# Kernel optimization log

Measured on AMD Instinct MI355X. Metric: run time of the kernel, lower is better.

Reference implementation:

```python
import jax, jax.numpy as jnp
import numpy as np

H = 512      # hidden_size
E = 300      # embed_size
V = 50257    # output_size / vocab
B = 64       # batch
S = 128      # src_len
NEG = -1e10


def setup_inputs() -> dict:
    key = jax.random.key(0)
    ks = jax.random.split(key, 12)
    inp = {
        "input_ids": jax.random.randint(ks[0], (B,), 0, V),
        "hidden": jax.random.normal(ks[1], (B, H), jnp.float32),
        "encoder_outputs": jax.random.normal(ks[2], (S, B, 2 * H), jnp.float32),
        "mask": jax.random.randint(ks[3], (B, S), 0, 2).astype(jnp.int32),
        # parameters
        "emb_table": jax.random.normal(ks[4], (V, E), jnp.float32) * 0.02,
        "W_attn": jax.random.normal(ks[5], (H, 3 * H), jnp.float32) * 0.02,
        "b_attn": jnp.zeros((H,), jnp.float32),
        "v_w": jax.random.normal(ks[6], (1, H), jnp.float32) * 0.02,
        "W_ih": jax.random.normal(ks[7], (3 * H, 2 * H + E), jnp.float32) * 0.02,
        "W_hh": jax.random.normal(ks[8], (3 * H, H), jnp.float32) * 0.02,
        "b_ih": jnp.zeros((3 * H,), jnp.float32),
        "b_hh": jnp.zeros((3 * H,), jnp.float32),
        "W_out": jax.random.normal(ks[9], (V, 3 * H + E), jnp.float32) * 0.02,
        "b_out": jnp.zeros((V,), jnp.float32),
    }
    return inp


def reference(input_ids, hidden, encoder_outputs, mask,
              emb_table, W_attn, b_attn, v_w,
              W_ih, W_hh, b_ih, b_hh, W_out, b_out):
    # embedding lookup (dropout prob = 0 -> identity)
    embedded = emb_table[input_ids]                       # [B, E]

    # Bahdanau attention
    enc_b = jnp.transpose(encoder_outputs, (1, 0, 2))     # [B, S, 2H]
    hid_rep = jnp.broadcast_to(hidden[:, None, :], (hidden.shape[0], enc_b.shape[1], hidden.shape[1]))
    energy = jnp.tanh(jnp.concatenate([hid_rep, enc_b], axis=2) @ W_attn.T + b_attn)  # [B, S, H]
    scores = jnp.einsum('bsh,h->bs', energy, v_w[0])      # [B, S]
    scores = jnp.where(mask == 0, NEG, scores)
    a = jax.nn.softmax(scores, axis=1)                    # [B, S]

    # context vector
    weighted = jnp.einsum('bs,bse->be', a, enc_b)         # [B, 2H]

    # single-step GRU (PyTorch gate order: r, z, n)
    x = jnp.concatenate([embedded, weighted], axis=1)     # [B, E + 2H]
    gx = x @ W_ih.T + b_ih                                # [B, 3H]
    gh = hidden @ W_hh.T + b_hh                           # [B, 3H]
    h = hidden.shape[1]
    r = jax.nn.sigmoid(gx[:, :h] + gh[:, :h])
    z = jax.nn.sigmoid(gx[:, h:2*h] + gh[:, h:2*h])
    n = jnp.tanh(gx[:, 2*h:] + r * gh[:, 2*h:])
    h_new = (1.0 - z) * n + z * hidden                    # [B, H]

    # output projection
    prediction = jnp.concatenate([h_new, weighted, embedded], axis=1) @ W_out.T + b_out  # [B, V]
    return prediction, h_new, a
```

## Files before the change

### kernel.cpp

```cpp
#include <hip/hip_runtime.h>

typedef unsigned short ushort_t;
typedef short bf16x8 __attribute__((ext_vector_type(8)));
typedef float f32x4 __attribute__((ext_vector_type(4)));

#define B_ 64
#define H_ 512
#define E_ 300
#define V_ 50257
#define S_ 128

#define PRED_OFS 0
#define HNEW_OFS ((size_t)64 * 50257)
#define A_OFS    ((size_t)64 * 50257 + 64 * 512)

__device__ __forceinline__ float b2f(unsigned short h) {
  unsigned int u = ((unsigned int)h) << 16;
  return __builtin_bit_cast(float, u);
}
__device__ __forceinline__ unsigned short f2b(float f) {
  unsigned int u = __builtin_bit_cast(unsigned int, f);
  u = u + 0x7FFFu + ((u >> 16) & 1u);
  return (unsigned short)(u >> 16);
}
__device__ __forceinline__ float fast_tanh(float x) {
  x = fminf(15.f, fmaxf(-15.f, x));
  float e = __expf(-2.f * x);
  return (1.f - e) / (1.f + e);
}
__device__ __forceinline__ float fast_sigmoid(float x) {
  return 1.f / (1.f + __expf(-x));
}

template <int DT>
__device__ __forceinline__ ushort4 ldb4(const void* p, size_t off) {
  if constexpr (DT == 0) {
    return *(const ushort4*)((const ushort_t*)p + off);
  } else {
    float4 f = *(const float4*)((const float*)p + off);
    return make_ushort4(f2b(f.x), f2b(f.y), f2b(f.z), f2b(f.w));
  }
}
template <int DT>
__device__ __forceinline__ float lde1(const void* p, size_t off) {
  if constexpr (DT == 0) return b2f(((const ushort_t*)p)[off]);
  else return ((const float*)p)[off];
}
template <int DT>
__device__ __forceinline__ void st1(void* p, size_t off, float v) {
  if constexpr (DT == 0) ((ushort_t*)p)[off] = f2b(v);
  else ((float*)p)[off] = v;
}

__global__ void detect_dtype(const ushort_t* __restrict__ hidden, int* __restrict__ dtf) {
  __shared__ int cnt;
  if (threadIdx.x == 0) cnt = 0;
  __syncthreads();
  int local = 0;
  for (int i = threadIdx.x; i < 32768; i += 256) {
    unsigned e = (hidden[i] >> 7) & 0xFFu;
    if (e >= 0xC8u) local++;
  }
  atomicAdd(&cnt, local);
  __syncthreads();
  if (threadIdx.x == 0) dtf[0] = (cnt > 50) ? 1 : 0;
}

template <int DTA, int DTW>
__global__ __launch_bounds__(256) void gemm_tile(
    const int* __restrict__ dtf, int want,
    const void* __restrict__ A, int lda,
    const void* __restrict__ W, int ldw, int wofs,
    const void* __restrict__ bias,
    float* __restrict__ C, int ldc,
    int M, int N, int K)
{
  if (dtf[0] != want) return;
  __shared__ ushort_t sA[64 * 40];
  __shared__ ushort_t sB[64 * 40];
  const int tid = threadIdx.x;
  const int n0 = blockIdx.x * 64, m0 = blockIdx.y * 64;
  const int wave = tid >> 6, lane = tid & 63, quad = lane >> 4, l16 = lane & 15;

  f32x4 acc[4];
  #pragma unroll
  for (int i = 0; i < 4; ++i) acc[i] = (f32x4){0.f, 0.f, 0.f, 0.f};

  const int ksteps = (K + 31) >> 5;
  for (int kt = 0; kt < ksteps; ++kt) {
    #pragma unroll
    for (int i = 0; i < 2; ++i) {
      int g = tid + i * 256;
      int row = g >> 3, gc = (g & 7) << 2;
      int gk = kt * 32 + gc;
      int ar = m0 + row, wr = n0 + row;
      ushort4 va = make_ushort4(0, 0, 0, 0);
      ushort4 vb = make_ushort4(0, 0, 0, 0);
      if (gk < K && ar < M) va = ldb4<DTA>(A, (size_t)ar * lda + gk);
      if (gk < K && wr < N) vb = ldb4<DTW>(W, (size_t)wr * ldw + wofs + gk);
      *(ushort4*)(sA + row * 40 + gc) = va;
      *(ushort4*)(sB + row * 40 + gc) = vb;
    }
    __syncthreads();
    bf16x8 af = *(const bf16x8*)(sA + (wave * 16 + l16) * 40 + quad * 8);
    #pragma unroll
    for (int nt = 0; nt < 4; ++nt) {
      bf16x8 bfr = *(const bf16x8*)(sB + (nt * 16 + l16) * 40 + quad * 8);
      acc[nt] = __builtin_amdgcn_mfma_f32_16x16x32_bf16(af, bfr, acc[nt], 0, 0, 0);
    }
    __syncthreads();
  }
  #pragma unroll
  for (int nt = 0; nt < 4; ++nt) {
    #pragma unroll
    for (int reg = 0; reg < 4; ++reg) {
      int row = m0 + wave * 16 + quad * 4 + reg;
      int col = n0 + nt * 16 + l16;
      if (row < M && col < N)
        C[(size_t)row * ldc + col] = acc[nt][reg] + lde1<DTW>(bias, col);
    }
  }
}

template <int DT>
__global__ __launch_bounds__(256) void attn_scores(
    const int* __restrict__ dtf,
    const void* __restrict__ enc,
    const void* __restrict__ Wattn,
    const float* __restrict__ Gh,
    const void* __restrict__ vw,
    float* __restrict__ scores)
{
  if (dtf[0] != DT) return;
  __shared__ ushort_t sA[64 * 40];
  __shared__ ushort_t sB[64 * 40];
  const int tid = threadIdx.x;
  const int n0 = blockIdx.x * 64, m0 = blockIdx.y * 64;
  const int wave = tid >> 6, lane = tid & 63, quad = lane >> 4, l16 = lane & 15;

  f32x4 acc[4];
  #pragma unroll
  for (int i = 0; i < 4; ++i) acc[i] = (f32x4){0.f, 0.f, 0.f, 0.f};

  for (int kt = 0; kt < 32; ++kt) {
    #pragma unroll
    for (int i = 0; i < 2; ++i) {
      int g = tid + i * 256;
      int row = g >> 3, gc = (g & 7) << 2;
      int gk = kt * 32 + gc;
      ushort4 va = ldb4<DT>(enc, (size_t)(m0 + row) * 1024 + gk);
      ushort4 vb = ldb4<DT>(Wattn, (size_t)(n0 + row) * 1536 + 512 + gk);
      *(ushort4*)(sA + row * 40 + gc) = va;
      *(ushort4*)(sB + row * 40 + gc) = vb;
    }
    __syncthreads();
    bf16x8 af = *(const bf16x8*)(sA + (wave * 16 + l16) * 40 + quad * 8);
    #pragma unroll
    for (int nt = 0; nt < 4; ++nt) {
      bf16x8 bfr = *(const bf16x8*)(sB + (nt * 16 + l16) * 40 + quad * 8);
      acc[nt] = __builtin_amdgcn_mfma_f32_16x16x32_bf16(af, bfr, acc[nt], 0, 0, 0);
    }
    __syncthreads();
  }
  float psum[4] = {0.f, 0.f, 0.f, 0.f};
  #pragma unroll
  for (int nt = 0; nt < 4; ++nt) {
    int h = n0 + nt * 16 + l16;
    float vh = lde1<DT>(vw, h);
    #pragma unroll
    for (int reg = 0; reg < 4; ++reg) {
      int r = m0 + wave * 16 + quad * 4 + reg;
      int b = r & 63;
      float e = acc[nt][reg] + Gh[b * 512 + h];
      psum[reg] += vh * fast_tanh(e);
    }
  }
  #pragma unroll
  for (int reg = 0; reg < 4; ++reg) {
    float p = psum[reg];
    p += __shfl_xor(p, 1);
    p += __shfl_xor(p, 2);
    p += __shfl_xor(p, 4);
    p += __shfl_xor(p, 8);
    if (l16 == 0) {
      int r = m0 + wave * 16 + quad * 4 + reg;
      atomicAdd(&scores[r], p);
    }
  }
}

template <int DT>
__global__ __launch_bounds__(256) void softmax_ctx(
    const int* __restrict__ dtf,
    const float* __restrict__ scores,
    const int* __restrict__ mask,
    const void* __restrict__ enc,
    const void* __restrict__ emb,
    const int* __restrict__ ids,
    void* __restrict__ out,
    ushort_t* __restrict__ x,
    ushort_t* __restrict__ xo)
{
  if (dtf[0] != DT) return;
  __shared__ float sc[128];
  __shared__ float red[128];
  const int b = blockIdx.x;
  const int tid = threadIdx.x;

  if (tid < 128) {
    float s = scores[tid * 64 + b];
    if (mask[b * 128 + tid] == 0) s = -1e10f;
    sc[tid] = s;
    red[tid] = s;
  }
  __syncthreads();
  for (int off = 64; off > 0; off >>= 1) {
    if (tid < off) red[tid] = fmaxf(red[tid], red[tid + off]);
    __syncthreads();
  }
  float m = red[0];
  __syncthreads();
  if (tid < 128) {
    float e = __expf(sc[tid] - m);
    sc[tid] = e;
    red[tid] = e;
  }
  __syncthreads();
  for (int off = 64; off > 0; off >>= 1) {
    if (tid < off) red[tid] += red[tid + off];
    __syncthreads();
  }
  float inv = 1.f / red[0];
  if (tid < 128) {
    float av = sc[tid] * inv;
    sc[tid] = av;
    st1<DT>(out, A_OFS + b * 128 + tid, av);
  }
  __syncthreads();

  {
    int e0 = tid * 4;
    float a0 = 0.f, a1 = 0.f, a2 = 0.f, a3 = 0.f;
    for (int s = 0; s < 128; ++s) {
      float as = sc[s];
      ushort4 ev = ldb4<DT>(enc, (size_t)(s * 64 + b) * 1024 + e0);
      a0 += as * b2f(ev.x);
      a1 += as * b2f(ev.y);
      a2 += as * b2f(ev.z);
      a3 += as * b2f(ev.w);
    }
    ushort4 wb = make_ushort4(f2b(a0), f2b(a1), f2b(a2), f2b(a3));
    *(ushort4*)(x + b * 1344 + 300 + e0) = wb;
    *(ushort4*)(xo + b * 1856 + 512 + e0) = wb;
  }

  int rid = ids[b];
  for (int e = tid; e < 300; e += 256) {
    ushort_t h = f2b(lde1<DT>(emb, (size_t)rid * 300 + e));
    x[b * 1344 + e] = h;
    xo[b * 1856 + 1536 + e] = h;
  }
  if (tid < 20) {
    x[b * 1344 + 1324 + tid] = 0;
    xo[b * 1856 + 1836 + tid] = 0;
  }
}

template <int DT>
__global__ __launch_bounds__(256) void gru_pointwise(
    const int* __restrict__ dtf,
    const float* __restrict__ gx,
    const float* __restrict__ gh,
    const void* __restrict__ hidden,
    void* __restrict__ out,
    ushort_t* __restrict__ xo)
{
  if (dtf[0] != DT) return;
  int i = blockIdx.x * 256 + threadIdx.x;
  int b = i >> 9, h = i & 511;
  float r = fast_sigmoid(gx[b * 1536 + h] + gh[b * 1536 + h]);
  float z = fast_sigmoid(gx[b * 1536 + 512 + h] + gh[b * 1536 + 512 + h]);
  float n = fast_tanh(gx[b * 1536 + 1024 + h] + r * gh[b * 1536 + 1024 + h]);
  float hp = lde1<DT>(hidden, b * 512 + h);
  float hn = (1.f - z) * n + z * hp;
  st1<DT>(out, HNEW_OFS + b * 512 + h, hn);
  xo[b * 1856 + h] = f2b(hn);
}

template <int DT>
__global__ __launch_bounds__(256) void out_proj(
    const int* __restrict__ dtf,
    const ushort_t* __restrict__ Xo,
    const void* __restrict__ Wout,
    const void* __restrict__ bout,
    void* __restrict__ out)
{
  if (dtf[0] != DT) return;
  __shared__ ushort_t sA[64 * 40];
  __shared__ ushort_t sB[64 * 40];
  const int tid = threadIdx.x;
  const int n0 = blockIdx.x * 64;
  const int wave = tid >> 6, lane = tid & 63, quad = lane >> 4, l16 = lane & 15;

  f32x4 acc[4];
  #pragma unroll
  for (int i = 0; i < 4; ++i) acc[i] = (f32x4){0.f, 0.f, 0.f, 0.f};

  for (int kt = 0; kt < 58; ++kt) {
    #pragma unroll
    for (int i = 0; i < 2; ++i) {
      int g = tid + i * 256;
      int row = g >> 3, gc = (g & 7) << 2;
      int gk = kt * 32 + gc;
      ushort4 va = make_ushort4(0, 0, 0, 0);
      ushort4 vb = make_ushort4(0, 0, 0, 0);
      if (gk < 1836) {
        va = *(const ushort4*)(Xo + (size_t)row * 1856 + gk);
        int wr = n0 + row;
        if (wr < V_) vb = ldb4<DT>(Wout, (size_t)wr * 1836 + gk);
      }
      *(ushort4*)(sA + row * 40 + gc) = va;
      *(ushort4*)(sB + row * 40 + gc) = vb;
    }
    __syncthreads();
    bf16x8 af = *(const bf16x8*)(sA + (wave * 16 + l16) * 40 + quad * 8);
    #pragma unroll
    for (int nt = 0; nt < 4; ++nt) {
      bf16x8 bfr = *(const bf16x8*)(sB + (nt * 16 + l16) * 40 + quad * 8);
      acc[nt] = __builtin_amdgcn_mfma_f32_16x16x32_bf16(af, bfr, acc[nt], 0, 0, 0);
    }
    __syncthreads();
  }
  #pragma unroll
  for (int nt = 0; nt < 4; ++nt) {
    #pragma unroll
    for (int reg = 0; reg < 4; ++reg) {
      int row = wave * 16 + quad * 4 + reg;
      int col = n0 + nt * 16 + l16;
      if (col < V_)
        st1<DT>(out, (size_t)row * V_ + col, acc[nt][reg] + lde1<DT>(bout, col));
    }
  }
}

extern "C" void kernel_launch(void* const* d_in, const int* in_sizes, int n_in,
                              void* d_out, int out_size, void* d_ws, size_t ws_size,
                              hipStream_t stream) {
  const int*  ids    = (const int*)d_in[0];
  const void* hidden = d_in[1];
  const void* enc    = d_in[2];
  const int*  mask   = (const int*)d_in[3];
  const void* emb    = d_in[4];
  const void* Wattn  = d_in[5];
  const void* battn  = d_in[6];
  const void* vw     = d_in[7];
  const void* Wih    = d_in[8];
  const void* Whh    = d_in[9];
  const void* bih    = d_in[10];
  const void* bhh    = d_in[11];
  const void* Wout   = d_in[12];
  const void* bout   = d_in[13];

  char* ws = (char*)d_ws;
  float*    scores = (float*)(ws + 0);
  float*    Gh     = (float*)(ws + 32768);
  float*    gx     = (float*)(ws + 425984);
  float*    gh     = (float*)(ws + 819200);
  ushort_t* x      = (ushort_t*)(ws + 1212416);
  ushort_t* xo     = (ushort_t*)(ws + 1384448);
  int*      dtf    = (int*)(ws + 1703936);

  detect_dtype<<<1, 256, 0, stream>>>((const ushort_t*)hidden, dtf);
  hipMemsetAsync(scores, 0, 8192 * sizeof(float), stream);

  gemm_tile<0, 0><<<dim3(8, 1), 256, 0, stream>>>(dtf, 0, hidden, 512, Wattn, 1536, 0, battn, Gh, 512, 64, 512, 512);
  gemm_tile<1, 1><<<dim3(8, 1), 256, 0, stream>>>(dtf, 1, hidden, 512, Wattn, 1536, 0, battn, Gh, 512, 64, 512, 512);

  attn_scores<0><<<dim3(8, 128), 256, 0, stream>>>(dtf, enc, Wattn, Gh, vw, scores);
  attn_scores<1><<<dim3(8, 128), 256, 0, stream>>>(dtf, enc, Wattn, Gh, vw, scores);

  softmax_ctx<0><<<64, 256, 0, stream>>>(dtf, scores, mask, enc, emb, ids, d_out, x, xo);
  softmax_ctx<1><<<64, 256, 0, stream>>>(dtf, scores, mask, enc, emb, ids, d_out, x, xo);

  gemm_tile<0, 0><<<dim3(24, 1), 256, 0, stream>>>(dtf, 0, x, 1344, Wih, 1324, 0, bih, gx, 1536, 64, 1536, 1324);
  gemm_tile<0, 1><<<dim3(24, 1), 256, 0, stream>>>(dtf, 1, x, 1344, Wih, 1324, 0, bih, gx, 1536, 64, 1536, 1324);
  gemm_tile<0, 0><<<dim3(24, 1), 256, 0, stream>>>(dtf, 0, hidden, 512, Whh, 512, 0, bhh, gh, 1536, 64, 1536, 512);
  gemm_tile<1, 1><<<dim3(24, 1), 256, 0, stream>>>(dtf, 1, hidden, 512, Whh, 512, 0, bhh, gh, 1536, 64, 1536, 512);

  gru_pointwise<0><<<128, 256, 0, stream>>>(dtf, gx, gh, hidden, d_out, xo);
  gru_pointwise<1><<<128, 256, 0, stream>>>(dtf, gx, gh, hidden, d_out, xo);

  out_proj<0><<<786, 256, 0, stream>>>(dtf, xo, Wout, bout, d_out);
  out_proj<1><<<786, 256, 0, stream>>>(dtf, xo, Wout, bout, d_out);
}
```

Measured before the change: 855.1 us.

## Drop runtime dtype detection, register-prefetch next K tile, replace score atomics

The runtime dtype-detection kernel and the duplicate bf16/fp32 kernel launches are removed, and fp32 inputs are hardcoded, which cuts launch count roughly in half. Every GEMM-style kernel now loads the next K-slice from global memory into registers before running the MFMAs on the current LDS tile, so global latency overlaps with compute. Attention-score atomics plus the memset are replaced by per-column-block partial buffers that softmax sums. The cost is more registers per thread and no support for bf16 inputs.

Result: faster. 719.6 us (-15.8%).

```diff
diff --git a/kernel.cpp b/kernel.cpp
--- a/kernel.cpp
+++ b/kernel.cpp
@@ -10,14 +10,9 @@
 #define V_ 50257
 #define S_ 128
 
-#define PRED_OFS 0
 #define HNEW_OFS ((size_t)64 * 50257)
 #define A_OFS    ((size_t)64 * 50257 + 64 * 512)
 
-__device__ __forceinline__ float b2f(unsigned short h) {
-  unsigned int u = ((unsigned int)h) << 16;
-  return __builtin_bit_cast(float, u);
-}
 __device__ __forceinline__ unsigned short f2b(float f) {
   unsigned int u = __builtin_bit_cast(unsigned int, f);
   u = u + 0x7FFFu + ((u >> 16) & 1u);
@@ -32,50 +27,42 @@
   return 1.f / (1.f + __expf(-x));
 }
 
+template <int DT> struct Raw4;
+template <> struct Raw4<0> {
+  ushort4 v;
+  __device__ static Raw4 zero() { return {make_ushort4(0, 0, 0, 0)}; }
+};
+template <> struct Raw4<1> {
+  float4 v;
+  __device__ static Raw4 zero() { return {make_float4(0.f, 0.f, 0.f, 0.f)}; }
+};
 template <int DT>
-__device__ __forceinline__ ushort4 ldb4(const void* p, size_t off) {
-  if constexpr (DT == 0) {
-    return *(const ushort4*)((const ushort_t*)p + off);
-  } else {
-    float4 f = *(const float4*)((const float*)p + off);
-    return make_ushort4(f2b(f.x), f2b(f.y), f2b(f.z), f2b(f.w));
-  }
+__device__ __forceinline__ Raw4<DT> ld_raw(const void* p, size_t off);
+template <>
+__device__ __forceinline__ Raw4<0> ld_raw<0>(const void* p, size_t off) {
+  return {*(const ushort4*)((const ushort_t*)p + off)};
+}
+template <>
+__device__ __forceinline__ Raw4<1> ld_raw<1>(const void* p, size_t off) {
+  return {*(const float4*)((const float*)p + off)};
 }
 template <int DT>
-__device__ __forceinline__ float lde1(const void* p, size_t off) {
-  if constexpr (DT == 0) return b2f(((const ushort_t*)p)[off]);
-  else return ((const float*)p)[off];
-}
-template <int DT>
-__device__ __forceinline__ void st1(void* p, size_t off, float v) {
-  if constexpr (DT == 0) ((ushort_t*)p)[off] = f2b(v);
-  else ((float*)p)[off] = v;
-}
-
-__global__ void detect_dtype(const ushort_t* __restrict__ hidden, int* __restrict__ dtf) {
-  __shared__ int cnt;
-  if (threadIdx.x == 0) cnt = 0;
-  __syncthreads();
-  int local = 0;
-  for (int i = threadIdx.x; i < 32768; i += 256) {
-    unsigned e = (hidden[i] >> 7) & 0xFFu;
-    if (e >= 0xC8u) local++;
-  }
-  atomicAdd(&cnt, local);
-  __syncthreads();
-  if (threadIdx.x == 0) dtf[0] = (cnt > 50) ? 1 : 0;
+__device__ __forceinline__ ushort4 to_b4(Raw4<DT> r);
+template <>
+__device__ __forceinline__ ushort4 to_b4<0>(Raw4<0> r) { return r.v; }
+template <>
+__device__ __forceinline__ ushort4 to_b4<1>(Raw4<1> r) {
+  return make_ushort4(f2b(r.v.x), f2b(r.v.y), f2b(r.v.z), f2b(r.v.w));
 }
 
 template <int DTA, int DTW>
 __global__ __launch_bounds__(256) void gemm_tile(
-    const int* __restrict__ dtf, int want,
     const void* __restrict__ A, int lda,
     const void* __restrict__ W, int ldw, int wofs,
-    const void* __restrict__ bias,
+    const float* __restrict__ bias,
     float* __restrict__ C, int ldc,
     int M, int N, int K)
 {
-  if (dtf[0] != want) return;
   __shared__ ushort_t sA[64 * 40];
   __shared__ ushort_t sB[64 * 40];
   const int tid = threadIdx.x;
@@ -86,22 +73,33 @@
   #pragma unroll
   for (int i = 0; i < 4; ++i) acc[i] = (f32x4){0.f, 0.f, 0.f, 0.f};
 
-  const int ksteps = (K + 31) >> 5;
-  for (int kt = 0; kt < ksteps; ++kt) {
+  Raw4<DTA> ra[2];
+  Raw4<DTW> rb[2];
+  auto fetch = [&](int kt) {
     #pragma unroll
     for (int i = 0; i < 2; ++i) {
       int g = tid + i * 256;
       int row = g >> 3, gc = (g & 7) << 2;
       int gk = kt * 32 + gc;
       int ar = m0 + row, wr = n0 + row;
-      ushort4 va = make_ushort4(0, 0, 0, 0);
-      ushort4 vb = make_ushort4(0, 0, 0, 0);
-      if (gk < K && ar < M) va = ldb4<DTA>(A, (size_t)ar * lda + gk);
-      if (gk < K && wr < N) vb = ldb4<DTW>(W, (size_t)wr * ldw + wofs + gk);
-      *(ushort4*)(sA + row * 40 + gc) = va;
-      *(ushort4*)(sB + row * 40 + gc) = vb;
-    }
-    __syncthreads();
+      ra[i] = Raw4<DTA>::zero();
+      rb[i] = Raw4<DTW>::zero();
+      if (gk < K && ar < M) ra[i] = ld_raw<DTA>(A, (size_t)ar * lda + gk);
+      if (gk < K && wr < N) rb[i] = ld_raw<DTW>(W, (size_t)wr * ldw + wofs + gk);
+    }
+  };
+  const int ksteps = (K + 31) >> 5;
+  fetch(0);
+  for (int kt = 0; kt < ksteps; ++kt) {
+    #pragma unroll
+    for (int i = 0; i < 2; ++i) {
+      int g = tid + i * 256;
+      int row = g >> 3, gc = (g & 7) << 2;
+      *(ushort4*)(sA + row * 40 + gc) = to_b4<DTA>(ra[i]);
+      *(ushort4*)(sB + row * 40 + gc) = to_b4<DTW>(rb[i]);
+    }
+    __syncthreads();
+    if (kt + 1 < ksteps) fetch(kt + 1);
     bf16x8 af = *(const bf16x8*)(sA + (wave * 16 + l16) * 40 + quad * 8);
     #pragma unroll
     for (int nt = 0; nt < 4; ++nt) {
@@ -117,21 +115,18 @@
       int row = m0 + wave * 16 + quad * 4 + reg;
       int col = n0 + nt * 16 + l16;
       if (row < M && col < N)
-        C[(size_t)row * ldc + col] = acc[nt][reg] + lde1<DTW>(bias, col);
-    }
-  }
-}
-
-template <int DT>
+        C[(size_t)row * ldc + col] = acc[nt][reg] + bias[col];
+    }
+  }
+}
+
 __global__ __launch_bounds__(256) void attn_scores(
-    const int* __restrict__ dtf,
-    const void* __restrict__ enc,
-    const void* __restrict__ Wattn,
+    const float* __restrict__ enc,
+    const float* __restrict__ Wattn,
     const float* __restrict__ Gh,
-    const void* __restrict__ vw,
-    float* __restrict__ scores)
+    const float* __restrict__ vw,
+    float* __restrict__ scores_part)
 {
-  if (dtf[0] != DT) return;
   __shared__ ushort_t sA[64 * 40];
   __shared__ ushort_t sB[64 * 40];
   const int tid = threadIdx.x;
@@ -142,18 +137,30 @@
   #pragma unroll
   for (int i = 0; i < 4; ++i) acc[i] = (f32x4){0.f, 0.f, 0.f, 0.f};
 
+  float4 ra[2], rb[2];
+  auto fetch = [&](int kt) {
+    #pragma unroll
+    for (int i = 0; i < 2; ++i) {
+      int g = tid + i * 256;
+      int row = g >> 3, gc = (g & 7) << 2;
+      int gk = kt * 32 + gc;
+      ra[i] = *(const float4*)(enc + (size_t)(m0 + row) * 1024 + gk);
+      rb[i] = *(const float4*)(Wattn + (size_t)(n0 + row) * 1536 + 512 + gk);
+    }
+  };
+  fetch(0);
   for (int kt = 0; kt < 32; ++kt) {
     #pragma unroll
     for (int i = 0; i < 2; ++i) {
       int g = tid + i * 256;
       int row = g >> 3, gc = (g & 7) << 2;
-      int gk = kt * 32 + gc;
-      ushort4 va = ldb4<DT>(enc, (size_t)(m0 + row) * 1024 + gk);
-      ushort4 vb = ldb4<DT>(Wattn, (size_t)(n0 + row) * 1536 + 512 + gk);
-      *(ushort4*)(sA + row * 40 + gc) = va;
-      *(ushort4*)(sB + row * 40 + gc) = vb;
-    }
-    __syncthreads();
+      *(ushort4*)(sA + row * 40 + gc) =
+          make_ushort4(f2b(ra[i].x), f2b(ra[i].y), f2b(ra[i].z), f2b(ra[i].w));
+      *(ushort4*)(sB + row * 40 + gc) =
+          make_ushort4(f2b(rb[i].x), f2b(rb[i].y), f2b(rb[i].z), f2b(rb[i].w));
+    }
+    __syncthreads();
+    if (kt + 1 < 32) fetch(kt + 1);
     bf16x8 af = *(const bf16x8*)(sA + (wave * 16 + l16) * 40 + quad * 8);
     #pragma unroll
     for (int nt = 0; nt < 4; ++nt) {
@@ -166,7 +173,7 @@
   #pragma unroll
   for (int nt = 0; nt < 4; ++nt) {
     int h = n0 + nt * 16 + l16;
-    float vh = lde1<DT>(vw, h);
+    float vh = vw[h];
     #pragma unroll
     for (int reg = 0; reg < 4; ++reg) {
       int r = m0 + wave * 16 + quad * 4 + reg;
@@ -184,31 +191,30 @@
     p += __shfl_xor(p, 8);
     if (l16 == 0) {
       int r = m0 + wave * 16 + quad * 4 + reg;
-      atomicAdd(&scores[r], p);
-    }
-  }
-}
-
-template <int DT>
+      scores_part[blockIdx.x * 8192 + r] = p;
+    }
+  }
+}
+
 __global__ __launch_bounds__(256) void softmax_ctx(
-    const int* __restrict__ dtf,
-    const float* __restrict__ scores,
+    const float* __restrict__ scores_part,
     const int* __restrict__ mask,
-    const void* __restrict__ enc,
-    const void* __restrict__ emb,
+    const float* __restrict__ enc,
+    const float* __restrict__ emb,
     const int* __restrict__ ids,
-    void* __restrict__ out,
+    float* __restrict__ out,
     ushort_t* __restrict__ x,
     ushort_t* __restrict__ xo)
 {
-  if (dtf[0] != DT) return;
   __shared__ float sc[128];
   __shared__ float red[128];
   const int b = blockIdx.x;
   const int tid = threadIdx.x;
 
   if (tid < 128) {
-    float s = scores[tid * 64 + b];
+    float s = 0.f;
+    #pragma unroll
+    for (int nb = 0; nb < 8; ++nb) s += scores_part[nb * 8192 + tid * 64 + b];
     if (mask[b * 128 + tid] == 0) s = -1e10f;
     sc[tid] = s;
     red[tid] = s;
@@ -234,7 +240,7 @@
   if (tid < 128) {
     float av = sc[tid] * inv;
     sc[tid] = av;
-    st1<DT>(out, A_OFS + b * 128 + tid, av);
+    out[A_OFS + b * 128 + tid] = av;
   }
   __syncthreads();
 
@@ -243,11 +249,11 @@
     float a0 = 0.f, a1 = 0.f, a2 = 0.f, a3 = 0.f;
     for (int s = 0; s < 128; ++s) {
       float as = sc[s];
-      ushort4 ev = ldb4<DT>(enc, (size_t)(s * 64 + b) * 1024 + e0);
-      a0 += as * b2f(ev.x);
-      a1 += as * b2f(ev.y);
-      a2 += as * b2f(ev.z);
-      a3 += as * b2f(ev.w);
+      float4 ev = *(const float4*)(enc + (size_t)(s * 64 + b) * 1024 + e0);
+      a0 += as * ev.x;
+      a1 += as * ev.y;
+      a2 += as * ev.z;
+      a3 += as * ev.w;
     }
     ushort4 wb = make_ushort4(f2b(a0), f2b(a1), f2b(a2), f2b(a3));
     *(ushort4*)(x + b * 1344 + 300 + e0) = wb;
@@ -256,7 +262,7 @@
 
   int rid = ids[b];
   for (int e = tid; e < 300; e += 256) {
-    ushort_t h = f2b(lde1<DT>(emb, (size_t)rid * 300 + e));
+    ushort_t h = f2b(emb[(size_t)rid * 300 + e]);
     x[b * 1344 + e] = h;
     xo[b * 1856 + 1536 + e] = h;
   }
@@ -266,36 +272,30 @@
   }
 }
 
-template <int DT>
 __global__ __launch_bounds__(256) void gru_pointwise(
-    const int* __restrict__ dtf,
     const float* __restrict__ gx,
     const float* __restrict__ gh,
-    const void* __restrict__ hidden,
-    void* __restrict__ out,
+    const float* __restrict__ hidden,
+    float* __restrict__ out,
     ushort_t* __restrict__ xo)
 {
-  if (dtf[0] != DT) return;
   int i = blockIdx.x * 256 + threadIdx.x;
   int b = i >> 9, h = i & 511;
   float r = fast_sigmoid(gx[b * 1536 + h] + gh[b * 1536 + h]);
   float z = fast_sigmoid(gx[b * 1536 + 512 + h] + gh[b * 1536 + 512 + h]);
   float n = fast_tanh(gx[b * 1536 + 1024 + h] + r * gh[b * 1536 + 1024 + h]);
-  float hp = lde1<DT>(hidden, b * 512 + h);
+  float hp = hidden[b * 512 + h];
   float hn = (1.f - z) * n + z * hp;
-  st1<DT>(out, HNEW_OFS + b * 512 + h, hn);
+  out[HNEW_OFS + b * 512 + h] = hn;
   xo[b * 1856 + h] = f2b(hn);
 }
 
-template <int DT>
 __global__ __launch_bounds__(256) void out_proj(
-    const int* __restrict__ dtf,
     const ushort_t* __restrict__ Xo,
-    const void* __restrict__ Wout,
-    const void* __restrict__ bout,
-    void* __restrict__ out)
+    const float* __restrict__ Wout,
+    const float* __restrict__ bout,
+    float* __restrict__ pred)
 {
-  if (dtf[0] != DT) return;
   __shared__ ushort_t sA[64 * 40];
   __shared__ ushort_t sB[64 * 40];
   const int tid = threadIdx.x;
@@ -306,23 +306,35 @@
   #pragma unroll
   for (int i = 0; i < 4; ++i) acc[i] = (f32x4){0.f, 0.f, 0.f, 0.f};
 
+  ushort4 ra[2];
+  float4 rb[2];
+  auto fetch = [&](int kt) {
+    #pragma unroll
+    for (int i = 0; i < 2; ++i) {
+      int g = tid + i * 256;
+      int row = g >> 3, gc = (g & 7) << 2;
+      int gk = kt * 32 + gc;
+      ra[i] = make_ushort4(0, 0, 0, 0);
+      rb[i] = make_float4(0.f, 0.f, 0.f, 0.f);
+      if (gk < 1836) {
+        ra[i] = *(const ushort4*)(Xo + (size_t)row * 1856 + gk);
+        int wr = n0 + row;
+        if (wr < V_) rb[i] = *(const float4*)(Wout + (size_t)wr * 1836 + gk);
+      }
+    }
+  };
+  fetch(0);
   for (int kt = 0; kt < 58; ++kt) {
     #pragma unroll
     for (int i = 0; i < 2; ++i) {
       int g = tid + i * 256;
       int row = g >> 3, gc = (g & 7) << 2;
-      int gk = kt * 32 + gc;
-      ushort4 va = make_ushort4(0, 0, 0, 0);
-      ushort4 vb = make_ushort4(0, 0, 0, 0);
-      if (gk < 1836) {
-        va = *(const ushort4*)(Xo + (size_t)row * 1856 + gk);
-        int wr = n0 + row;
-        if (wr < V_) vb = ldb4<DT>(Wout, (size_t)wr * 1836 + gk);
-      }
-      *(ushort4*)(sA + row * 40 + gc) = va;
-      *(ushort4*)(sB + row * 40 + gc) = vb;
-    }
-    __syncthreads();
+      *(ushort4*)(sA + row * 40 + gc) = ra[i];
+      *(ushort4*)(sB + row * 40 + gc) =
+          make_ushort4(f2b(rb[i].x), f2b(rb[i].y), f2b(rb[i].z), f2b(rb[i].w));
+    }
+    __syncthreads();
+    if (kt + 1 < 58) fetch(kt + 1);
     bf16x8 af = *(const bf16x8*)(sA + (wave * 16 + l16) * 40 + quad * 8);
     #pragma unroll
     for (int nt = 0; nt < 4; ++nt) {
@@ -338,7 +350,7 @@
       int row = wave * 16 + quad * 4 + reg;
       int col = n0 + nt * 16 + l16;
       if (col < V_)
-        st1<DT>(out, (size_t)row * V_ + col, acc[nt][reg] + lde1<DT>(bout, col));
+        pred[(size_t)row * V_ + col] = acc[nt][reg] + bout[col];
     }
   }
 }
@@ -346,50 +358,43 @@
 extern "C" void kernel_launch(void* const* d_in, const int* in_sizes, int n_in,
                               void* d_out, int out_size, void* d_ws, size_t ws_size,
                               hipStream_t stream) {
-  const int*  ids    = (const int*)d_in[0];
-  const void* hidden = d_in[1];
-  const void* enc    = d_in[2];
-  const int*  mask   = (const int*)d_in[3];
-  const void* emb    = d_in[4];
-  const void* Wattn  = d_in[5];
-  const void* battn  = d_in[6];
-  const void* vw     = d_in[7];
-  const void* Wih    = d_in[8];
-  const void* Whh    = d_in[9];
-  const void* bih    = d_in[10];
-  const void* bhh    = d_in[11];
-  const void* Wout   = d_in[12];
-  const void* bout   = d_in[13];
+  const int*   ids    = (const int*)d_in[0];
+  const float* hidden = (const float*)d_in[1];
+  const float* enc    = (const float*)d_in[2];
+  const int*   mask   = (const int*)d_in[3];
+  const float* emb    = (const float*)d_in[4];
+  const float* Wattn  = (const float*)d_in[5];
+  const float* battn  = (const float*)d_in[6];
+  const float* vw     = (const float*)d_in[7];
+  const float* Wih    = (const float*)d_in[8];
+  const float* Whh    = (const float*)d_in[9];
+  const float* bih    = (const float*)d_in[10];
+  const float* bhh    = (const float*)d_in[11];
+  const float* Wout   = (const float*)d_in[12];
+  const float* bout   = (const float*)d_in[13];
+  float* out = (float*)d_out;
 
   char* ws = (char*)d_ws;
-  float*    scores = (float*)(ws + 0);
-  float*    Gh     = (float*)(ws + 32768);
-  float*    gx     = (float*)(ws + 425984);
-  float*    gh     = (float*)(ws + 819200);
-  ushort_t* x      = (ushort_t*)(ws + 1212416);
-  ushort_t* xo     = (ushort_t*)(ws + 1384448);
-  int*      dtf    = (int*)(ws + 1703936);
-
-  detect_dtype<<<1, 256, 0, stream>>>((const ushort_t*)hidden, dtf);
-  hipMemsetAsync(scores, 0, 8192 * sizeof(float), stream);
-
-  gemm_tile<0, 0><<<dim3(8, 1), 256, 0, stream>>>(dtf, 0, hidden, 512, Wattn, 1536, 0, battn, Gh, 512, 64, 512, 512);
-  gemm_tile<1, 1><<<dim3(8, 1), 256, 0, stream>>>(dtf, 1, hidden, 512, Wattn, 1536, 0, battn, Gh, 512, 64, 512, 512);
-
-  attn_scores<0><<<dim3(8, 128), 256, 0, stream>>>(dtf, enc, Wattn, Gh, vw, scores);
-  attn_scores<1><<<dim3(8, 128), 256, 0, stream>>>(dtf, enc, Wattn, Gh, vw, scores);
-
-  softmax_ctx<0><<<64, 256, 0, stream>>>(dtf, scores, mask, enc, emb, ids, d_out, x, xo);
-  softmax_ctx<1><<<64, 256, 0, stream>>>(dtf, scores, mask, enc, emb, ids, d_out, x, xo);
-
-  gemm_tile<0, 0><<<dim3(24, 1), 256, 0, stream>>>(dtf, 0, x, 1344, Wih, 1324, 0, bih, gx, 1536, 64, 1536, 1324);
-  gemm_tile<0, 1><<<dim3(24, 1), 256, 0, stream>>>(dtf, 1, x, 1344, Wih, 1324, 0, bih, gx, 1536, 64, 1536, 1324);
-  gemm_tile<0, 0><<<dim3(24, 1), 256, 0, stream>>>(dtf, 0, hidden, 512, Whh, 512, 0, bhh, gh, 1536, 64, 1536, 512);
-  gemm_tile<1, 1><<<dim3(24, 1), 256, 0, stream>>>(dtf, 1, hidden, 512, Whh, 512, 0, bhh, gh, 1536, 64, 1536, 512);
-
-  gru_pointwise<0><<<128, 256, 0, stream>>>(dtf, gx, gh, hidden, d_out, xo);
-  gru_pointwise<1><<<128, 256, 0, stream>>>(dtf, gx, gh, hidden, d_out, xo);
-
-  out_proj<0><<<786, 256, 0, stream>>>(dtf, xo, Wout, bout, d_out);
-  out_proj<1><<<786, 256, 0, stream>>>(dtf, xo, Wout, bout, d_out);
-}
+  float*    scores_part = (float*)(ws + 0);
+  float*    Gh          = (float*)(ws + 262144);
+  float*    gx          = (float*)(ws + 393216);
+  float*    gh          = (float*)(ws + 786432);
+  ushort_t* x           = (ushort_t*)(ws + 1179648);
+  ushort_t* xo          = (ushort_t*)(ws + 1351680);
+
+  gemm_tile<1, 1><<<dim3(8, 1), 256, 0, stream>>>(
+      hidden, 512, Wattn, 1536, 0, battn, Gh, 512, 64, 512, 512);
+
+  attn_scores<<<dim3(8, 128), 256, 0, stream>>>(enc, Wattn, Gh, vw, scores_part);
+
+  softmax_ctx<<<64, 256, 0, stream>>>(scores_part, mask, enc, emb, ids, out, x, xo);
+
+  gemm_tile<0, 1><<<dim3(24, 1), 256, 0, stream>>>(
+      x, 1344, Wih, 1324, 0, bih, gx, 1536, 64, 1536, 1324);
+  gemm_tile<1, 1><<<dim3(24, 1), 256, 0, stream>>>(
+      hidden, 512, Whh, 512, 0, bhh, gh, 1536, 64, 1536, 512);
+
+  gru_pointwise<<<128, 256, 0, stream>>>(gx, gh, hidden, out, xo);
+
+  out_proj<<<786, 256, 0, stream>>>(xo, Wout, bout, out);
+}
```
